# Kernel tuning notes

Hardware: AMD Instinct MI355X
Metric: run time of the kernel (lower is better)

The kernel has to match this reference:

```python
import jax, jax.numpy as jnp
import numpy as np

N, IN_DIM, OUT_DIM, HEADS = 2048, 512, 512, 8
HEAD_DIM = OUT_DIM // HEADS
NEG_SLOPE = 0.2


def setup_inputs() -> dict:
    key = jax.random.key(0)
    k1, k2, k3, k4 = jax.random.split(key, 4)
    x = jax.random.normal(k1, (N, IN_DIM), dtype=jnp.float32)
    adj = jax.random.randint(k2, (N, N), 0, 2, dtype=jnp.int32)
    W = jax.random.normal(k3, (IN_DIM, OUT_DIM), dtype=jnp.float32) * 0.02
    a = jax.random.normal(k4, (2 * HEAD_DIM,), dtype=jnp.float32) * 0.02
    return {"x": x, "adj": adj, "W": W, "a": a}


def reference(x, adj, W, a):
    # Wh: (N, H, Dh)
    Wh = (x @ W).reshape(N, HEADS, HEAD_DIM)
    # a . concat(Wh_i, Wh_j) == (Wh_i . a_src) + (Wh_j . a_dst) -- exact decomposition,
    # avoids materializing the (N, N, H, 2*Dh) concat tensor.
    a_src, a_dst = a[:HEAD_DIM], a[HEAD_DIM:]
    s_i = jnp.einsum('nhd,d->nh', Wh, a_src)  # contribution of dest node i
    s_j = jnp.einsum('nhd,d->nh', Wh, a_dst)  # contribution of source node j
    e = jax.nn.leaky_relu(s_i[:, None, :] + s_j[None, :, :], negative_slope=NEG_SLOPE)  # (N, N, H)
    mask = (adj > 0)[:, :, None]
    e = jnp.where(mask, e, jnp.float32(-jnp.inf))
    alpha = jax.nn.softmax(e, axis=1)  # softmax over source nodes j
    # out[i,h,:] = sum_j alpha[i,j,h] * Wh[j,h,:]   (dropout is identity at eval)
    out = jnp.einsum('ijh,jhd->ihd', alpha, Wh)
    return out.reshape(N, OUT_DIM)
```

## Files before the change

### kernel.cpp

```cpp
#include <hip/hip_runtime.h>
#include <hip/hip_bf16.h>

#define NN 2048
#define KD 512
#define ODIM 512
#define NHEAD 8
#define HD 64
#define NEG 0.2f

typedef float f32x4 __attribute__((ext_vector_type(4)));
typedef short bf16x8 __attribute__((ext_vector_type(8)));
typedef short bf16x4 __attribute__((ext_vector_type(4)));
typedef unsigned int u32x4 __attribute__((ext_vector_type(4)));
typedef unsigned long long u64;
typedef unsigned int u32;

__device__ __forceinline__ short tob(float f) {
  __hip_bfloat16 h = __float2bfloat16(f);
  return *reinterpret_cast<short*>(&h);
}

__device__ __forceinline__ void gl_lds16(const void* g, void* l) {
  __builtin_amdgcn_global_load_lds(
      (const __attribute__((address_space(1))) u32*)g,
      (__attribute__((address_space(3))) u32*)l, 16, 0, 0);
}

__device__ __forceinline__ u32 to_lds(const void* p) {
  return (u32)(size_t)(const __attribute__((address_space(3))) char*)p;
}

#define DSR(dst, addr, OFFLIT)                      \
  asm volatile("ds_read_b128 %0, %1 offset:" OFFLIT \
               : "=v"(dst)                          \
               : "v"(addr))

__global__ __launch_bounds__(256) void prep(const float* __restrict__ X,
                                            const float* __restrict__ W,
                                            const int* __restrict__ adj,
                                            short* __restrict__ Xf,
                                            short* __restrict__ Bf,
                                            unsigned short* __restrict__ bits) {
  __shared__ float sbuf[16 * 516];
  const int b = blockIdx.x;
  const int t = threadIdx.x;

  if (b < 1024) {
    const int T = b * 256 + t;
    const int row = T >> 7, g = T & 127;
    const int* p = adj + (size_t)row * NN + g * 16;
    u32 m = 0;
#pragma unroll
    for (int q = 0; q < 4; ++q) {
      const int4 v = *(const int4*)&p[q * 4];
      m |= (v.x > 0 ? 1u : 0u) << (q * 4);
      m |= (v.y > 0 ? 2u : 0u) << (q * 4);
      m |= (v.z > 0 ? 4u : 0u) << (q * 4);
      m |= (v.w > 0 ? 8u : 0u) << (q * 4);
    }
    bits[T] = (unsigned short)m;
    return;
  }

  if (b < 1024 + 128) {
    const int xb = b - 1024;
#pragma unroll
    for (int q = 0; q < 8; ++q) {
      const int flat = q * 256 + t;
      const int row = flat >> 7, c4 = flat & 127;
      const float4 v = *(const float4*)&X[(size_t)(xb * 16 + row) * KD + c4 * 4];
      *(float4*)&sbuf[row * 516 + c4 * 4] = v;
    }
    __syncthreads();
#pragma unroll
    for (int c = 0; c < 4; ++c) {
      const int s = c * 256 + t;
      const int l = s & 63;
      const int col = l & 15, kg = (l >> 4) & 3;
      const int k0 = (s >> 6) * 32 + kg * 8;
      bf16x8 o;
#pragma unroll
      for (int u = 0; u < 8; ++u) o[u] = tob(sbuf[col * 516 + k0 + u]);
      *(bf16x8*)&Xf[((size_t)xb * 1024 + s) * 8] = o;
    }
    return;
  }

  const int b2 = b - 1152;
  const int kb = b2 & 7, h = b2 >> 3;
  const int k0 = kb * 64;
#pragma unroll
  for (int q = 0; q < 4; ++q) {
    const int flat = q * 256 + t;
    const int kk = flat >> 4, o4 = (flat & 15) * 4;
    const float4 v = *(const float4*)&W[(size_t)(k0 + kk) * ODIM + h * 64 + o4];
    *(float4*)&sbuf[kk * 68 + o4] = v;
  }
  __syncthreads();
#pragma unroll
  for (int c = 0; c < 2; ++c) {
    const int s = c * 256 + t;
    const int ksl = s >> 8, nt = (s >> 6) & 3, l = s & 63;
    const int col = l & 15, kg = (l >> 4) & 3;
    const int kloc = ksl * 32 + kg * 8;
    const int od = nt * 16 + col;
    bf16x8 o;
#pragma unroll
    for (int u = 0; u < 8; ++u) o[u] = tob(sbuf[(kloc + u) * 68 + od]);
    const size_t off = (((size_t)(h * 4 + nt) * 16 + kb * 2 + ksl) * 64 + l) * 8;
    *(bf16x8*)&Bf[off] = o;
  }
}

__global__ __launch_bounds__(256) void gemm_fused(
    const short* __restrict__ Xf, const short* __restrict__ Bf,
    const float* __restrict__ a, short* __restrict__ WhF,
    float2* __restrict__ esrcp, u32* __restrict__ edstp) {
  __shared__ float pbuf[4 * 4 * 64 * 4];
  const int t = threadIdx.x;
  const int lane = t & 63, w = t >> 6;
  const int col = lane & 15, kgrp = lane >> 4;
  const int bx = blockIdx.x;
  const int h = blockIdx.y;
  const int i0 = bx * 32;

  {
    const int mtg = bx * 2 + (w & 1);
    const int kh = w >> 1;
    const short* ax = Xf + (size_t)mtg * 8192;
    const short* bxp = Bf + (size_t)h * 32768;

    f32x4 acc1[4] = {};
#pragma unroll
    for (int k2 = 0; k2 < 8; ++k2) {
      const int ks = kh * 8 + k2;
      const bf16x8 af = *(const bf16x8*)&ax[(ks * 64 + lane) * 8];
#pragma unroll
      for (int nt = 0; nt < 4; ++nt) {
        const bf16x8 bf = *(const bf16x8*)&bxp[((nt * 16 + ks) * 64 + lane) * 8];
        acc1[nt] = __builtin_amdgcn_mfma_f32_16x16x32_bf16(af, bf, acc1[nt], 0, 0, 0);
      }
    }
#pragma unroll
    for (int nt = 0; nt < 4; ++nt)
      *(f32x4*)&pbuf[((w * 4 + nt) * 64 + lane) * 4] = acc1[nt];
  }
  __syncthreads();

  if (w < 2) {
    f32x4 acc[4];
#pragma unroll
    for (int nt = 0; nt < 4; ++nt) {
      const f32x4 p0 = *(const f32x4*)&pbuf[((w * 4 + nt) * 64 + lane) * 4];
      const f32x4 p1 = *(const f32x4*)&pbuf[(((w + 2) * 4 + nt) * 64 + lane) * 4];
      acc[nt] = p0 + p1;
    }
    float asv[4], adv[4];
#pragma unroll
    for (int nt = 0; nt < 4; ++nt) {
      asv[nt] = a[nt * 16 + col];
      adv[nt] = a[64 + nt * 16 + col];
    }
    float ps[4], pd[4];
#pragma unroll
    for (int r = 0; r < 4; ++r) {
      float s1 = 0.f, s2 = 0.f;
#pragma unroll
      for (int nt = 0; nt < 4; ++nt) {
        s1 += acc[nt][r] * asv[nt];
        s2 += acc[nt][r] * adv[nt];
      }
      ps[r] = s1;
      pd[r] = s2;
    }
#pragma unroll
    for (int off = 1; off <= 8; off <<= 1) {
#pragma unroll
      for (int r = 0; r < 4; ++r) {
        ps[r] += __shfl_xor(ps[r], off);
        pd[r] += __shfl_xor(pd[r], off);
      }
    }
    {
      const size_t tbase = ((size_t)h * 32 + (bx >> 1)) * 4096;
      const int lp = (w * 2 + (kgrp >> 1)) * 16 + col;
      const int u0 = (kgrp & 1) * 4;
      const int slot_ks = bx & 1;
#pragma unroll
      for (int nt = 0; nt < 4; ++nt) {
        bf16x4 o;
#pragma unroll
        for (int r = 0; r < 4; ++r) o[r] = tob(acc[nt][r]);
        *(bf16x4*)&WhF[tbase + (size_t)(nt * 2 + slot_ks) * 512 + lp * 8 + u0] = o;
      }
    }
    if (col == 0) {
      const int mbase = i0 + w * 16 + kgrp * 4;
#pragma unroll
      for (int r = 0; r < 4; ++r) {
        const int n = mbase + r;
        esrcp[h * NN + n] = make_float2(__expf(ps[r]), __expf(NEG * ps[r]));
        const u32 lo = (u32)(unsigned short)tob(__expf(pd[r]));
        const u32 hi = (u32)(unsigned short)tob(__expf(NEG * pd[r]));
        edstp[h * NN + n] = (hi << 16) | lo;
      }
    }
  }
}

__global__ __launch_bounds__(512, 4) void attn_mfma(
    const short* __restrict__ WhF, const unsigned char* __restrict__ adjbits,
    const float2* __restrict__ esrcp, const u32* __restrict__ edstp,
    float* __restrict__ out) {
  extern __shared__ __align__(16) char smem[];
  const int t = threadIdx.x;
  const int lane = t & 63;
  const int wid = t >> 6;
  const int jq = wid & 3;
  const int mh = wid >> 2;
  const int col = lane & 15, kgrp = lane >> 4;
  const int h = blockIdx.y;
  const int i0 = blockIdx.x * 32;
  const int irow = i0 + mh * 16;

  char* qbase = smem + jq * 18432;
  char* dbuf = qbase;
  char* elds = qbase + 16384;

  const short* tb = WhF + ((size_t)h * 32 + jq * 8) * 4096;
  const int jb = jq * 512;

  const float2 e0 = esrcp[h * NN + irow + col];
  const float A0 = e0.x, C0 = e0.y;

  u64 aw[8];
  {
    const unsigned char* rb = adjbits + (size_t)(irow + col) * (NN / 8) + jq * 64;
#pragma unroll
    for (int q = 0; q < 4; ++q) {
      const uint4 v = *(const uint4*)(rb + q * 16);
      aw[q * 2] = (u64)v.x | ((u64)v.y << 32);
      aw[q * 2 + 1] = (u64)v.z | ((u64)v.w << 32);
    }
  }

  bf16x8 ones;
#pragma unroll
  for (int u = 0; u < 8; ++u) ones[u] = (short)0x3F80;

  f32x4 acc[4] = {};
  f32x4 accd = {};

  const u32 lread = to_lds(dbuf) + (u32)lane * 16u;
  const u32 eread = to_lds(elds) + (u32)kgrp * 32u;

  {
    gl_lds16(edstp + h * NN + jb + mh * 256 + lane * 4, elds + mh * 1024);
#pragma unroll
    for (int s = 0; s < 4; ++s) {
      const int slot = mh * 4 + s;
      gl_lds16(tb + slot * 512 + lane * 8, dbuf + slot * 1024);
    }
  }

#pragma unroll
  for (int tt = 0; tt < 8; ++tt) {
    const int cur = tt & 1, nxt = cur ^ 1;

    if (tt < 7) {
      const short* g = tb + (size_t)(tt + 1) * 4096;
      char* sb = dbuf + nxt * 8192;
#pragma unroll
      for (int s = 0; s < 4; ++s) {
        const int slot = mh * 4 + s;
        gl_lds16(g + slot * 512 + lane * 8, sb + slot * 1024);
      }
      asm volatile("s_waitcnt vmcnt(4)" ::: "memory");
    } else {
      asm volatile("s_waitcnt vmcnt(0)" ::: "memory");
    }
    __builtin_amdgcn_sched_barrier(0);
    __builtin_amdgcn_s_barrier();

    const u32 abuf = lread + (u32)(cur * 8192);
    bf16x8 b0, b1, b2, b3, b4, b5, b6, b7;
    DSR(b0, abuf, "0");
    DSR(b1, abuf, "1024");
    DSR(b2, abuf, "2048");
    DSR(b3, abuf, "3072");
    DSR(b4, abuf, "4096");
    DSR(b5, abuf, "5120");
    DSR(b6, abuf, "6144");
    DSR(b7, abuf, "7168");
    u32x4 eq[4];
    switch (tt) {
      case 0: DSR(eq[0], eread, "0");    DSR(eq[1], eread, "16");   DSR(eq[2], eread, "128");  DSR(eq[3], eread, "144");  break;
      case 1: DSR(eq[0], eread, "256");  DSR(eq[1], eread, "272");  DSR(eq[2], eread, "384");  DSR(eq[3], eread, "400");  break;
      case 2: DSR(eq[0], eread, "512");  DSR(eq[1], eread, "528");  DSR(eq[2], eread, "640");  DSR(eq[3], eread, "656");  break;
      case 3: DSR(eq[0], eread, "768");  DSR(eq[1], eread, "784");  DSR(eq[2], eread, "896");  DSR(eq[3], eread, "912");  break;
      case 4: DSR(eq[0], eread, "1024"); DSR(eq[1], eread, "1040"); DSR(eq[2], eread, "1152"); DSR(eq[3], eread, "1168"); break;
      case 5: DSR(eq[0], eread, "1280"); DSR(eq[1], eread, "1296"); DSR(eq[2], eread, "1408"); DSR(eq[3], eread, "1424"); break;
      case 6: DSR(eq[0], eread, "1536"); DSR(eq[1], eread, "1552"); DSR(eq[2], eread, "1664"); DSR(eq[3], eread, "1680"); break;
      default:DSR(eq[0], eread, "1792"); DSR(eq[1], eread, "1808"); DSR(eq[2], eread, "1920"); DSR(eq[3], eread, "1936"); break;
    }
    asm volatile("s_waitcnt lgkmcnt(0)" ::: "memory");
    __builtin_amdgcn_sched_barrier(0);

    bf16x8 af[2];
#pragma unroll
    for (int ks = 0; ks < 2; ++ks) {
      const u32 mb = (u32)(aw[tt] >> ((ks * 4 + kgrp) * 8)) & 0xffu;
      const u32x4 q0 = eq[ks * 2], q1 = eq[ks * 2 + 1];
      const u32 uw[8] = {q0[0], q0[1], q0[2], q0[3], q1[0], q1[1], q1[2], q1[3]};
#pragma unroll
      for (int u2 = 0; u2 < 8; ++u2) {
        const float B = __uint_as_float(uw[u2] << 16);
        const float D = __uint_as_float(uw[u2] & 0xffff0000u);
        float p = fmaxf(A0 * B, C0 * D);
        p = ((mb >> u2) & 1u) ? p : 0.f;
        af[ks][u2] = tob(p);
      }
    }

    __builtin_amdgcn_s_setprio(1);
    accd = __builtin_amdgcn_mfma_f32_16x16x32_bf16(af[0], ones, accd, 0, 0, 0);
    accd = __builtin_amdgcn_mfma_f32_16x16x32_bf16(af[1], ones, accd, 0, 0, 0);
    acc[0] = __builtin_amdgcn_mfma_f32_16x16x32_bf16(af[0], b0, acc[0], 0, 0, 0);
    acc[0] = __builtin_amdgcn_mfma_f32_16x16x32_bf16(af[1], b1, acc[0], 0, 0, 0);
    acc[1] = __builtin_amdgcn_mfma_f32_16x16x32_bf16(af[0], b2, acc[1], 0, 0, 0);
    acc[1] = __builtin_amdgcn_mfma_f32_16x16x32_bf16(af[1], b3, acc[1], 0, 0, 0);
    acc[2] = __builtin_amdgcn_mfma_f32_16x16x32_bf16(af[0], b4, acc[2], 0, 0, 0);
    acc[2] = __builtin_amdgcn_mfma_f32_16x16x32_bf16(af[1], b5, acc[2], 0, 0, 0);
    acc[3] = __builtin_amdgcn_mfma_f32_16x16x32_bf16(af[0], b6, acc[3], 0, 0, 0);
    acc[3] = __builtin_amdgcn_mfma_f32_16x16x32_bf16(af[1], b7, acc[3], 0, 0, 0);
    __builtin_amdgcn_s_setprio(0);

    __builtin_amdgcn_s_barrier();
  }

  __syncthreads();
  float* red = (float*)smem;
  float* rw = red + (size_t)((mh * 4 + jq) * 16) * 66;
#pragma unroll
  for (int nt = 0; nt < 4; ++nt)
#pragma unroll
    for (int r = 0; r < 4; ++r)
      rw[(kgrp * 4 + r) * 66 + nt * 16 + col] = acc[nt][r];
  if (col == 0) {
#pragma unroll
    for (int r = 0; r < 4; ++r) rw[(kgrp * 4 + r) * 66 + 64] = accd[r];
  }
  __syncthreads();

  const int d = t & 63, idx = t >> 6;
#pragma unroll
  for (int rr = 0; rr < 4; ++rr) {
    const int row = rr * 8 + idx;
    const int mh2 = row >> 4, r16 = row & 15;
    float v = 0.f, dd = 0.f;
#pragma unroll
    for (int q = 0; q < 4; ++q) {
      const float* rb = red + (size_t)((mh2 * 4 + q) * 16 + r16) * 66;
      v += rb[d];
      dd += rb[64];
    }
    out[(size_t)(i0 + row) * ODIM + h * HD + d] = v / dd;
  }
}

extern "C" void kernel_launch(void* const* d_in, const int* in_sizes, int n_in,
                              void* d_out, int out_size, void* d_ws,
                              size_t ws_size, hipStream_t stream) {
  const float* x = (const float*)d_in[0];
  const int* adj = (const int*)d_in[1];
  const float* W = (const float*)d_in[2];
  const float* a = (const float*)d_in[3];
  float* out = (float*)d_out;

  char* ws = (char*)d_ws;
  short* WhF = (short*)ws;
  short* Xf = (short*)(ws + (2 << 20));
  short* Bf = (short*)(ws + (4 << 20));
  unsigned short* bits =
      (unsigned short*)(ws + (4 << 20) + (512 << 10));
  float2* esrcp = (float2*)(ws + (5 << 20));
  u32* edstp = (u32*)(ws + (5 << 20) + (128 << 10));

  prep<<<1216, 256, 0, stream>>>(x, W, adj, Xf, Bf, bits);
  gemm_fused<<<dim3(64, 8), 256, 0, stream>>>(Xf, Bf, a, WhF, esrcp, edstp);
  attn_mfma<<<dim3(64, 8), 512, 73728, stream>>>(
      WhF, (const unsigned char*)bits, esrcp, edstp, out);
}
```

Baseline: 34.86 us.

## Move adjacency bit-packing into GEMM launch and split dest-exponent storage

The adjacency bit-packing blocks move out of the prep kernel and into the GEMM kernel as extra blocks. They can then run alongside the projection GEMM instead of delaying the conversion of X and W. The packed bf16 pair for the destination exponents is replaced by an fp32 array for exp(pd) plus a bf16 array for exp(0.2*pd), which keeps more precision in one term. The attention loop now issues its exponent LDS reads with compile-time offsets and waits partially so the probability computation overlaps the WhF tile reads. It also packs results with v_cvt_pk_bf16_f32, at the cost of more LDS per block.

After: 33.73 us. -3.3%, faster.

```diff
diff --git a/kernel.cpp b/kernel.cpp
--- a/kernel.cpp
+++ b/kernel.cpp
@@ -15,6 +15,11 @@
 typedef unsigned long long u64;
 typedef unsigned int u32;
 
+typedef union {
+  u32x4 w;
+  bf16x8 h;
+} pk8;
+
 __device__ __forceinline__ short tob(float f) {
   __hip_bfloat16 h = __float2bfloat16(f);
   return *reinterpret_cast<short*>(&h);
@@ -35,35 +40,18 @@
                : "=v"(dst)                          \
                : "v"(addr))
 
+#define QSTRIDE 19456
+
 __global__ __launch_bounds__(256) void prep(const float* __restrict__ X,
                                             const float* __restrict__ W,
-                                            const int* __restrict__ adj,
                                             short* __restrict__ Xf,
-                                            short* __restrict__ Bf,
-                                            unsigned short* __restrict__ bits) {
+                                            short* __restrict__ Bf) {
   __shared__ float sbuf[16 * 516];
   const int b = blockIdx.x;
   const int t = threadIdx.x;
 
-  if (b < 1024) {
-    const int T = b * 256 + t;
-    const int row = T >> 7, g = T & 127;
-    const int* p = adj + (size_t)row * NN + g * 16;
-    u32 m = 0;
-#pragma unroll
-    for (int q = 0; q < 4; ++q) {
-      const int4 v = *(const int4*)&p[q * 4];
-      m |= (v.x > 0 ? 1u : 0u) << (q * 4);
-      m |= (v.y > 0 ? 2u : 0u) << (q * 4);
-      m |= (v.z > 0 ? 4u : 0u) << (q * 4);
-      m |= (v.w > 0 ? 8u : 0u) << (q * 4);
-    }
-    bits[T] = (unsigned short)m;
-    return;
-  }
-
-  if (b < 1024 + 128) {
-    const int xb = b - 1024;
+  if (b < 128) {
+    const int xb = b;
 #pragma unroll
     for (int q = 0; q < 8; ++q) {
       const int flat = q * 256 + t;
@@ -86,7 +74,7 @@
     return;
   }
 
-  const int b2 = b - 1152;
+  const int b2 = b - 128;
   const int kb = b2 & 7, h = b2 >> 3;
   const int k0 = kb * 64;
 #pragma unroll
@@ -112,16 +100,37 @@
   }
 }
 
-__global__ __launch_bounds__(256) void gemm_fused(
+__global__ __launch_bounds__(256) void gemm_adj(
     const short* __restrict__ Xf, const short* __restrict__ Bf,
-    const float* __restrict__ a, short* __restrict__ WhF,
-    float2* __restrict__ esrcp, u32* __restrict__ edstp) {
+    const float* __restrict__ a, const int* __restrict__ adj,
+    short* __restrict__ WhF, float2* __restrict__ esrcp,
+    float* __restrict__ eB, unsigned short* __restrict__ eD,
+    unsigned short* __restrict__ bits) {
   __shared__ float pbuf[4 * 4 * 64 * 4];
+  const int b = blockIdx.x;
   const int t = threadIdx.x;
+
+  if (b >= 512) {
+    const int T = (b - 512) * 256 + t;
+    const int row = T >> 7, g = T & 127;
+    const int* p = adj + (size_t)row * NN + g * 16;
+    u32 m = 0;
+#pragma unroll
+    for (int q = 0; q < 4; ++q) {
+      const int4 v = *(const int4*)&p[q * 4];
+      m |= (v.x > 0 ? 1u : 0u) << (q * 4);
+      m |= (v.y > 0 ? 2u : 0u) << (q * 4);
+      m |= (v.z > 0 ? 4u : 0u) << (q * 4);
+      m |= (v.w > 0 ? 8u : 0u) << (q * 4);
+    }
+    bits[T] = (unsigned short)m;
+    return;
+  }
+
   const int lane = t & 63, w = t >> 6;
   const int col = lane & 15, kgrp = lane >> 4;
-  const int bx = blockIdx.x;
-  const int h = blockIdx.y;
+  const int bx = b & 63;
+  const int h = b >> 6;
   const int i0 = bx * 32;
 
   {
@@ -200,9 +209,8 @@
       for (int r = 0; r < 4; ++r) {
         const int n = mbase + r;
         esrcp[h * NN + n] = make_float2(__expf(ps[r]), __expf(NEG * ps[r]));
-        const u32 lo = (u32)(unsigned short)tob(__expf(pd[r]));
-        const u32 hi = (u32)(unsigned short)tob(__expf(NEG * pd[r]));
-        edstp[h * NN + n] = (hi << 16) | lo;
+        eB[h * NN + n] = __expf(pd[r]);
+        eD[h * NN + n] = (unsigned short)tob(__expf(NEG * pd[r]));
       }
     }
   }
@@ -210,8 +218,8 @@
 
 __global__ __launch_bounds__(512, 4) void attn_mfma(
     const short* __restrict__ WhF, const unsigned char* __restrict__ adjbits,
-    const float2* __restrict__ esrcp, const u32* __restrict__ edstp,
-    float* __restrict__ out) {
+    const float2* __restrict__ esrcp, const float* __restrict__ eB,
+    const unsigned short* __restrict__ eD, float* __restrict__ out) {
   extern __shared__ __align__(16) char smem[];
   const int t = threadIdx.x;
   const int lane = t & 63;
@@ -223,9 +231,10 @@
   const int i0 = blockIdx.x * 32;
   const int irow = i0 + mh * 16;
 
-  char* qbase = smem + jq * 18432;
+  char* qbase = smem + jq * QSTRIDE;
   char* dbuf = qbase;
-  char* elds = qbase + 16384;
+  char* eBl = qbase + 16384;
+  char* eDl = qbase + 18432;
 
   const short* tb = WhF + ((size_t)h * 32 + jq * 8) * 4096;
   const int jb = jq * 512;
@@ -252,10 +261,15 @@
   f32x4 accd = {};
 
   const u32 lread = to_lds(dbuf) + (u32)lane * 16u;
-  const u32 eread = to_lds(elds) + (u32)kgrp * 32u;
+  const u32 ereadB = to_lds(eBl) + (u32)kgrp * 32u;
+  const u32 ereadD = to_lds(eDl) + (u32)kgrp * 16u;
 
   {
-    gl_lds16(edstp + h * NN + jb + mh * 256 + lane * 4, elds + mh * 1024);
+    gl_lds16((const char*)eB + ((size_t)h * NN + jb) * 4 + mh * 1024 +
+                 lane * 16,
+             eBl + mh * 1024);
+    if (mh == 0)
+      gl_lds16((const char*)eD + ((size_t)h * NN + jb) * 2 + lane * 16, eDl);
 #pragma unroll
     for (int s = 0; s < 4; ++s) {
       const int slot = mh * 4 + s;
@@ -282,6 +296,15 @@
     __builtin_amdgcn_sched_barrier(0);
     __builtin_amdgcn_s_barrier();
 
+    const u32 erB = ereadB + (u32)(tt * 256);
+    const u32 erD = ereadD + (u32)(tt * 128);
+    u32x4 qb0, qb1, qb2, qb3, qd0, qd1;
+    DSR(qb0, erB, "0");
+    DSR(qb1, erB, "16");
+    DSR(qb2, erB, "128");
+    DSR(qb3, erB, "144");
+    DSR(qd0, erD, "0");
+    DSR(qd1, erD, "64");
     const u32 abuf = lread + (u32)(cur * 8192);
     bf16x8 b0, b1, b2, b3, b4, b5, b6, b7;
     DSR(b0, abuf, "0");
@@ -292,35 +315,41 @@
     DSR(b5, abuf, "5120");
     DSR(b6, abuf, "6144");
     DSR(b7, abuf, "7168");
-    u32x4 eq[4];
-    switch (tt) {
-      case 0: DSR(eq[0], eread, "0");    DSR(eq[1], eread, "16");   DSR(eq[2], eread, "128");  DSR(eq[3], eread, "144");  break;
-      case 1: DSR(eq[0], eread, "256");  DSR(eq[1], eread, "272");  DSR(eq[2], eread, "384");  DSR(eq[3], eread, "400");  break;
-      case 2: DSR(eq[0], eread, "512");  DSR(eq[1], eread, "528");  DSR(eq[2], eread, "640");  DSR(eq[3], eread, "656");  break;
-      case 3: DSR(eq[0], eread, "768");  DSR(eq[1], eread, "784");  DSR(eq[2], eread, "896");  DSR(eq[3], eread, "912");  break;
-      case 4: DSR(eq[0], eread, "1024"); DSR(eq[1], eread, "1040"); DSR(eq[2], eread, "1152"); DSR(eq[3], eread, "1168"); break;
-      case 5: DSR(eq[0], eread, "1280"); DSR(eq[1], eread, "1296"); DSR(eq[2], eread, "1408"); DSR(eq[3], eread, "1424"); break;
-      case 6: DSR(eq[0], eread, "1536"); DSR(eq[1], eread, "1552"); DSR(eq[2], eread, "1664"); DSR(eq[3], eread, "1680"); break;
-      default:DSR(eq[0], eread, "1792"); DSR(eq[1], eread, "1808"); DSR(eq[2], eread, "1920"); DSR(eq[3], eread, "1936"); break;
-    }
+
+    asm volatile("s_waitcnt lgkmcnt(8)" ::: "memory");
+    __builtin_amdgcn_sched_barrier(0);
+    bf16x8 af[2];
+#pragma unroll
+    for (int ks = 0; ks < 2; ++ks) {
+      const u32 mb = (u32)(aw[tt] >> ((ks * 4 + kgrp) * 8)) & 0xffu;
+      const u32x4 qlo = ks ? qb2 : qb0;
+      const u32x4 qhi = ks ? qb3 : qb1;
+      const u32x4 qd = ks ? qd1 : qd0;
+      float pv[8];
+#pragma unroll
+      for (int u2 = 0; u2 < 8; ++u2) {
+        const u32 bw = (u2 < 4) ? qlo[u2 & 3] : qhi[u2 & 3];
+        const float fB = __uint_as_float(bw);
+        const u32 dw = qd[u2 >> 1];
+        const float fD =
+            __uint_as_float((u2 & 1) ? (dw & 0xffff0000u) : (dw << 16));
+        const float p = fmaxf(A0 * fB, C0 * fD);
+        pv[u2] = ((mb >> u2) & 1u) ? p : 0.f;
+      }
+      pk8 r;
+#pragma unroll
+      for (int w2 = 0; w2 < 4; ++w2) {
+        u32 rr;
+        asm("v_cvt_pk_bf16_f32 %0, %1, %2"
+            : "=v"(rr)
+            : "v"(pv[w2 * 2]), "v"(pv[w2 * 2 + 1]));
+        r.w[w2] = rr;
+      }
+      af[ks] = r.h;
+    }
+
     asm volatile("s_waitcnt lgkmcnt(0)" ::: "memory");
     __builtin_amdgcn_sched_barrier(0);
-
-    bf16x8 af[2];
-#pragma unroll
-    for (int ks = 0; ks < 2; ++ks) {
-      const u32 mb = (u32)(aw[tt] >> ((ks * 4 + kgrp) * 8)) & 0xffu;
-      const u32x4 q0 = eq[ks * 2], q1 = eq[ks * 2 + 1];
-      const u32 uw[8] = {q0[0], q0[1], q0[2], q0[3], q1[0], q1[1], q1[2], q1[3]};
-#pragma unroll
-      for (int u2 = 0; u2 < 8; ++u2) {
-        const float B = __uint_as_float(uw[u2] << 16);
-        const float D = __uint_as_float(uw[u2] & 0xffff0000u);
-        float p = fmaxf(A0 * B, C0 * D);
-        p = ((mb >> u2) & 1u) ? p : 0.f;
-        af[ks][u2] = tob(p);
-      }
-    }
 
     __builtin_amdgcn_s_setprio(1);
     accd = __builtin_amdgcn_mfma_f32_16x16x32_bf16(af[0], ones, accd, 0, 0, 0);
@@ -384,10 +413,12 @@
   unsigned short* bits =
       (unsigned short*)(ws + (4 << 20) + (512 << 10));
   float2* esrcp = (float2*)(ws + (5 << 20));
-  u32* edstp = (u32*)(ws + (5 << 20) + (128 << 10));
-
-  prep<<<1216, 256, 0, stream>>>(x, W, adj, Xf, Bf, bits);
-  gemm_fused<<<dim3(64, 8), 256, 0, stream>>>(Xf, Bf, a, WhF, esrcp, edstp);
-  attn_mfma<<<dim3(64, 8), 512, 73728, stream>>>(
-      WhF, (const unsigned char*)bits, esrcp, edstp, out);
-}
+  float* eB = (float*)(ws + (5 << 20) + (128 << 10));
+  unsigned short* eD =
+      (unsigned short*)(ws + (5 << 20) + (192 << 10));
+
+  prep<<<192, 256, 0, stream>>>(x, W, Xf, Bf);
+  gemm_adj<<<1536, 256, 0, stream>>>(Xf, Bf, a, adj, WhF, esrcp, eB, eD, bits);
+  attn_mfma<<<dim3(64, 8), 512, 4 * QSTRIDE, stream>>>(
+      WhF, (const unsigned char*)bits, esrcp, eB, eD, out);
+}
```
